# Kernel optimization log

Hardware: AMD Instinct MI355X
Metric: run time of the kernel (lower is better)

Reference implementation:

```python
import jax, jax.numpy as jnp
import numpy as np

B, T, D = 2, 2048, 1024
H = 16
HD = D // H
SCALE = 1.0 / np.sqrt(HD).astype(np.float32)


def setup_inputs() -> dict:
    key = jax.random.key(0)
    ks = jax.random.split(key, 5)
    std = 1.0 / np.sqrt(D).astype(np.float32)
    x = jax.random.normal(ks[0], (B, T, D), dtype=jnp.float32)
    Wqkvt = jax.random.normal(ks[1], (D, 4 * D), dtype=jnp.float32) * std
    bqkvt = jax.random.normal(ks[2], (4 * D,), dtype=jnp.float32) * 0.02
    Wout = jax.random.normal(ks[3], (D, D), dtype=jnp.float32) * std
    bout = jax.random.normal(ks[4], (D,), dtype=jnp.float32) * 0.02
    return {"x": x, "Wqkvt": Wqkvt, "bqkvt": bqkvt, "Wout": Wout, "bout": bout}


def reference(x, Wqkvt, bqkvt, Wout, bout):
    b, t, d = x.shape
    # fused qkvt projection -> [B,T,4,H,HD]
    qkvt = (x @ Wqkvt + bqkvt).reshape(b, t, 4, H, HD)
    # -> [B,H,T,HD] each
    q, k, v, tt = [jnp.transpose(qkvt[:, :, i], (0, 2, 1, 3)) for i in range(4)]

    # standard dot-product scores [B,H,T,T]
    scores_dot = jnp.einsum('bhqd,bhkd->bhqk', q, k)
    # triplet term: (q*t) against cumsum over keys of (k*v)/sqrt(hd)
    kv = k * v * SCALE
    kv_cum = jnp.cumsum(kv, axis=2)  # causal prefix over key positions
    scores_trip = jnp.einsum('bhqd,bhkd->bhqk', q * tt, kv_cum)

    scores = (scores_dot + scores_trip) * SCALE
    causal = jnp.triu(jnp.ones((t, t), dtype=bool), k=1)
    scores = jnp.where(causal[None, None], -jnp.inf, scores)

    attn = jax.nn.softmax(scores, axis=-1)
    out = jnp.einsum('bhqk,bhkd->bhqd', attn, v)  # [B,H,T,HD]
    out = jnp.transpose(out, (0, 2, 1, 3)).reshape(b, t, d)
    return out @ Wout + bout
```

## Files before the change

### kernel.cpp

```cpp
#include <hip/hip_runtime.h>

#define T_SEQ 2048
#define D_MODEL 1024
#define NH 16
#define HD 64
#define BH_TOT 32
#define M_ROWS 4096
#define NT 32
#define SCALE 0.125f
#define BHT (BH_TOT * T_SEQ)
#define LOG2E 1.44269504f
#define TAU 2.885f

typedef _Float16 h8 __attribute__((ext_vector_type(8)));
typedef _Float16 h4 __attribute__((ext_vector_type(4)));
typedef float f32x4 __attribute__((ext_vector_type(4)));

__device__ __forceinline__ f32x4 mfma_h(h8 a, h8 b, f32x4 c) {
    return __builtin_amdgcn_mfma_f32_16x16x32_f16(a, b, c, 0, 0, 0);
}

__device__ __forceinline__ void gload16(const _Float16* g, _Float16* l) {
    __builtin_amdgcn_global_load_lds(
        (const __attribute__((address_space(1))) unsigned int*)g,
        (__attribute__((address_space(3))) unsigned int*)l, 16, 0, 0);
}

__global__ void k_convert(const float* __restrict__ in, _Float16* __restrict__ out, int n) {
    int i = (blockIdx.x * blockDim.x + threadIdx.x) * 4;
    if (i < n) {
        float4 v = *(const float4*)(in + i);
        h4 o;
        o[0] = (_Float16)v.x; o[1] = (_Float16)v.y;
        o[2] = (_Float16)v.z; o[3] = (_Float16)v.w;
        *(h4*)(out + i) = o;
    }
}

__global__ void k_transpose(const float* __restrict__ in, _Float16* __restrict__ out, int K, int N) {
    __shared__ float tile[32][33];
    int nb = blockIdx.x * 32, kb = blockIdx.y * 32;
    int tx = threadIdx.x & 31, ty = threadIdx.x >> 5;
    #pragma unroll
    for (int i = 0; i < 32; i += 8)
        tile[ty + i][tx] = in[(size_t)(kb + ty + i) * N + (nb + tx)];
    __syncthreads();
    #pragma unroll
    for (int i = 0; i < 32; i += 8)
        out[(size_t)(nb + ty + i) * K + (kb + tx)] = (_Float16)tile[tx][ty + i];
}

template<int MODE>
__launch_bounds__(256, 2)
__global__ void k_gemm(const _Float16* __restrict__ A, const _Float16* __restrict__ Bt,
                       int M, int N, int K, const float* __restrict__ bias,
                       _Float16* __restrict__ qo, _Float16* __restrict__ keo,
                       _Float16* __restrict__ vo, _Float16* __restrict__ vto,
                       _Float16* __restrict__ to, float* __restrict__ cOut)
{
    __shared__ __align__(16) _Float16 lA[2][128 * 64];
    __shared__ __align__(16) _Float16 lB[2][128 * 64];
    const int tid = threadIdx.x;
    const int wid = tid >> 6, lane = tid & 63, lrow = lane & 15, lg = lane >> 4;
    const int wm = wid >> 1, wn = wid & 1;
    const int m0 = blockIdx.x * 128, n0 = blockIdx.y * 128;

    f32x4 acc[4][4];
    #pragma unroll
    for (int i = 0; i < 4; i++)
        #pragma unroll
        for (int j = 0; j < 4; j++) acc[i][j] = (f32x4){0.f, 0.f, 0.f, 0.f};

    const int rin = lane >> 3, gcol = lane & 7;
    const int scol = (gcol ^ rin) * 8;
    const _Float16* gA = A + (size_t)(m0 + 32 * wid + rin) * K + scol;
    const _Float16* gB = Bt + (size_t)(n0 + 32 * wid + rin) * K + scol;

    const int r7 = lrow & 7;
    const int nk = K >> 6;

    #pragma unroll
    for (int i = 0; i < 4; i++) {
        gload16(gA + (size_t)(8 * i) * K, &lA[0][32 * wid * 64 + 8 * i * 64]);
        gload16(gB + (size_t)(8 * i) * K, &lB[0][32 * wid * 64 + 8 * i * 64]);
    }
    __syncthreads();

    for (int kt = 0; kt < nk; ++kt) {
        const int cur = kt & 1;
        if (kt + 1 < nk) {
            const size_t ko = (size_t)(kt + 1) * 64;
            #pragma unroll
            for (int i = 0; i < 4; i++) {
                gload16(gA + (size_t)(8 * i) * K + ko, &lA[cur ^ 1][32 * wid * 64 + 8 * i * 64]);
                gload16(gB + (size_t)(8 * i) * K + ko, &lB[cur ^ 1][32 * wid * 64 + 8 * i * 64]);
            }
        }
        h8 af[4][2], bfr[4][2];
        #pragma unroll
        for (int mi = 0; mi < 4; mi++) {
            const int row = wm * 64 + mi * 16 + lrow;
            af[mi][0] = *(const h8*)&lA[cur][row * 64 + ((lg ^ r7) * 8)];
            af[mi][1] = *(const h8*)&lA[cur][row * 64 + (((4 + lg) ^ r7) * 8)];
        }
        #pragma unroll
        for (int ni = 0; ni < 4; ni++) {
            const int row = wn * 64 + ni * 16 + lrow;
            bfr[ni][0] = *(const h8*)&lB[cur][row * 64 + ((lg ^ r7) * 8)];
            bfr[ni][1] = *(const h8*)&lB[cur][row * 64 + (((4 + lg) ^ r7) * 8)];
        }
        #pragma unroll
        for (int mi = 0; mi < 4; mi++)
            #pragma unroll
            for (int ni = 0; ni < 4; ni++) {
                acc[mi][ni] = mfma_h(af[mi][0], bfr[ni][0], acc[mi][ni]);
                acc[mi][ni] = mfma_h(af[mi][1], bfr[ni][1], acc[mi][ni]);
            }
        __syncthreads();
    }

    if (MODE == 0) {
        const int ssel = n0 >> 10;
        #pragma unroll
        for (int mi = 0; mi < 4; mi++) {
            #pragma unroll
            for (int ni = 0; ni < 4; ni++) {
                const int nn = n0 + wn * 64 + ni * 16 + lrow;
                const float bv = bias[nn];
                const int h = (nn >> 6) & 15, hd = nn & 63;
                const int mmb = m0 + wm * 64 + mi * 16 + 4 * lg;
                const int b = mmb >> 11, t0 = mmb & (T_SEQ - 1);
                const size_t rowb = (size_t)(b * NH + h) * T_SEQ;
                h4 hv;
                #pragma unroll
                for (int r = 0; r < 4; r++) hv[r] = (_Float16)(acc[mi][ni][r] + bv);
                if (ssel == 0) {
                    #pragma unroll
                    for (int r = 0; r < 4; r++) qo[(rowb + t0 + r) * HD + hd] = hv[r];
                } else if (ssel == 1) {
                    #pragma unroll
                    for (int r = 0; r < 4; r++) keo[(rowb + t0 + r) * 128 + hd] = hv[r];
                } else if (ssel == 2) {
                    #pragma unroll
                    for (int r = 0; r < 4; r++) vo[(rowb + t0 + r) * HD + hd] = hv[r];
                    *(h4*)&vto[((size_t)(b * NH + h) * HD + hd) * T_SEQ + t0] = hv;
                } else {
                    #pragma unroll
                    for (int r = 0; r < 4; r++) to[(rowb + t0 + r) * HD + hd] = hv[r];
                }
            }
        }
    } else {
        #pragma unroll
        for (int mi = 0; mi < 4; mi++) {
            #pragma unroll
            for (int ni = 0; ni < 4; ni++) {
                const int nn = n0 + wn * 64 + ni * 16 + lrow;
                const float bv = bias[nn];
                #pragma unroll
                for (int r = 0; r < 4; r++) {
                    const int mm = m0 + wm * 64 + mi * 16 + 4 * lg + r;
                    cOut[(size_t)mm * N + nn] = acc[mi][ni][r] + bv;
                }
            }
        }
    }
}

__global__ void k_kvcum(_Float16* __restrict__ Ke, const _Float16* __restrict__ Vb)
{
    const int bh = blockIdx.x;
    const int w = threadIdx.x >> 6, lane = threadIdx.x & 63;
    const size_t bk = (size_t)bh * T_SEQ * 128 + lane;
    const size_t bv = (size_t)bh * T_SEQ * HD + lane;
    const int CH = T_SEQ / 16;
    const int t0 = w * CH;
    float s = 0.f;
    for (int i = 0; i < CH; i++)
        s += (float)Ke[bk + (size_t)(t0 + i) * 128] * (float)Vb[bv + (size_t)(t0 + i) * HD];
    __shared__ float tot[16][64];
    tot[w][lane] = s;
    __syncthreads();
    float acc = 0.f;
    for (int ww = 0; ww < w; ww++) acc += tot[ww][lane];
    for (int i = 0; i < CH; i++) {
        size_t ok = bk + (size_t)(t0 + i) * 128;
        acc += (float)Ke[ok] * (float)Vb[bv + (size_t)(t0 + i) * HD];
        Ke[ok + 64] = (_Float16)(acc * SCALE);
    }
}

__launch_bounds__(256, 2)
__global__ void k_attn(const _Float16* __restrict__ Qb, const _Float16* __restrict__ Ke,
                       const _Float16* __restrict__ Vt, const _Float16* __restrict__ Tb,
                       _Float16* __restrict__ Op0, _Float16* __restrict__ Op1,
                       _Float16* __restrict__ Op2, _Float16* __restrict__ Op3,
                       float* __restrict__ ML, int nsplit)
{
    const int bh = blockIdx.x;
    const int pair = blockIdx.y;
    const int ksel = blockIdx.z;
    const int tid = threadIdx.x;
    const int wid = tid >> 6, lane = tid & 63, lrow = lane & 15, lg = lane >> 4;
    const _Float16* qp = Qb + (size_t)bh * T_SEQ * HD;
    const _Float16* kep = Ke + (size_t)bh * T_SEQ * 128;
    const _Float16* tp = Tb + (size_t)bh * T_SEQ * HD;
    const _Float16* vp = Vt + (size_t)bh * T_SEQ * HD;
    _Float16* op = (ksel == 0) ? Op0 : (ksel == 1) ? Op1 : (ksel == 2) ? Op2 : Op3;
    float* ml = ML + (size_t)ksel * BHT * 2;

    __shared__ __align__(16) _Float16 ldsK[2][64 * 128];
    __shared__ __align__(16) _Float16 ldsV[2][64 * 64];
    __shared__ __align__(16) _Float16 lP[4][16 * 64];

    const int r7 = lrow & 7;
    int kswz[4];
    #pragma unroll
    for (int c = 0; c < 4; c++) kswz[c] = ((c * 4 + lg) ^ r7) * 8;

    const int krow4 = lane >> 4, kg = lane & 15;
    const int vrow8 = lane >> 3, vg = lane & 7;
    auto stage = [&](int j, int buf) {
        #pragma unroll
        for (int rr = 0; rr < 4; rr++) {
            const int row = 16 * wid + rr * 4 + krow4;
            gload16(&kep[(size_t)(j * 64 + row) * 128 + ((kg ^ (row & 7)) * 8)],
                    &ldsK[buf][(16 * wid + rr * 4) * 128]);
        }
        #pragma unroll
        for (int rr = 0; rr < 2; rr++) {
            const int d = 16 * wid + rr * 8 + vrow8;
            gload16(&vp[(size_t)d * T_SEQ + j * 64 + ((vg ^ (d & 7)) * 8)],
                    &ldsV[buf][(16 * wid + rr * 8) * 64]);
        }
    };

    const h8 ones = {(_Float16)1.f, (_Float16)1.f, (_Float16)1.f, (_Float16)1.f,
                     (_Float16)1.f, (_Float16)1.f, (_Float16)1.f, (_Float16)1.f};
    const float C = SCALE * LOG2E;

    for (int half = 0; half < 2; ++half) {
        const int qi = half ? (NT - 1 - pair) : pair;
        const int q0 = qi * 64;
        const int nj = qi + 1;
        const int jbeg = (nj * ksel) / nsplit;
        const int jend = (nj * (ksel + 1)) / nsplit;

        const int qrow = q0 + wid * 16 + lrow;
        h8 qf[4];
        #pragma unroll
        for (int ks = 0; ks < 2; ++ks) {
            h8 qv = *(const h8*)&qp[(size_t)qrow * HD + ks * 32 + lg * 8];
            h8 tv = *(const h8*)&tp[(size_t)qrow * HD + ks * 32 + lg * 8];
            h8 a2, b2;
            #pragma unroll
            for (int i = 0; i < 8; i++) {
                float qq = (float)qv[i] * C;
                a2[i] = (_Float16)qq;
                b2[i] = (_Float16)(qq * (float)tv[i]);
            }
            qf[ks] = a2; qf[2 + ks] = b2;
        }

        float m_r[4];
        f32x4 o[4], o4;
        #pragma unroll
        for (int r = 0; r < 4; r++) m_r[r] = -__builtin_inff();
        #pragma unroll
        for (int ct = 0; ct < 4; ct++) o[ct] = (f32x4){0.f, 0.f, 0.f, 0.f};
        o4 = (f32x4){0.f, 0.f, 0.f, 0.f};

        if (jbeg < jend) stage(jbeg, 0);
        __syncthreads();

        for (int j = jbeg; j < jend; ++j) {
            const int cur = (j - jbeg) & 1;
            if (j + 1 < jend) stage(j + 1, cur ^ 1);

            f32x4 s[4];
            #pragma unroll
            for (int ct = 0; ct < 4; ct++) {
                const _Float16* kb = &ldsK[cur][(ct * 16 + lrow) * 128];
                f32x4 sv = (f32x4){0.f, 0.f, 0.f, 0.f};
                sv = mfma_h(qf[0], *(const h8*)&kb[kswz[0]], sv);
                sv = mfma_h(qf[1], *(const h8*)&kb[kswz[1]], sv);
                sv = mfma_h(qf[2], *(const h8*)&kb[kswz[2]], sv);
                sv = mfma_h(qf[3], *(const h8*)&kb[kswz[3]], sv);
                s[ct] = sv;
            }
            if (j == qi) {
                #pragma unroll
                for (int ct = 0; ct < 4; ct++)
                    #pragma unroll
                    for (int r = 0; r < 4; r++) {
                        int key = j * 64 + ct * 16 + lrow;
                        int qr  = q0 + wid * 16 + 4 * lg + r;
                        if (key > qr) s[ct][r] = -__builtin_inff();
                    }
            }
            float mx[4];
            #pragma unroll
            for (int r = 0; r < 4; r++)
                mx[r] = fmaxf(fmaxf(s[0][r], s[1][r]), fmaxf(s[2][r], s[3][r]));
            bool need = (mx[0] > m_r[0] + TAU) | (mx[1] > m_r[1] + TAU) |
                        (mx[2] > m_r[2] + TAU) | (mx[3] > m_r[3] + TAU);
            if (__any(need)) {
                #pragma unroll
                for (int d = 1; d < 16; d <<= 1)
                    #pragma unroll
                    for (int r = 0; r < 4; r++) mx[r] = fmaxf(mx[r], __shfl_xor(mx[r], d, 64));
                #pragma unroll
                for (int r = 0; r < 4; r++) {
                    float mn = fmaxf(m_r[r], mx[r]);
                    float scl = __builtin_amdgcn_exp2f(m_r[r] - mn);
                    o[0][r] *= scl; o[1][r] *= scl; o[2][r] *= scl; o[3][r] *= scl;
                    o4[r] *= scl;
                    m_r[r] = mn;
                }
            }
            #pragma unroll
            for (int ct = 0; ct < 4; ct++) {
                const int col = ct * 16 + lrow;
                #pragma unroll
                for (int r = 0; r < 4; r++) {
                    float p = __builtin_amdgcn_exp2f(s[ct][r] - m_r[r]);
                    const int row = 4 * lg + r;
                    const int boff = row * 128 + ((col * 2) ^ ((row & 7) << 4));
                    lP[wid][boff >> 1] = (_Float16)p;
                }
            }
            h8 pa[2];
            #pragma unroll
            for (int ks = 0; ks < 2; ks++) {
                const int boff = lrow * 128 + ((ks * 64 + lg * 16) ^ ((lrow & 7) << 4));
                pa[ks] = *(const h8*)((const char*)lP[wid] + boff);
            }
            o4 = mfma_h(pa[0], ones, o4);
            o4 = mfma_h(pa[1], ones, o4);
            #pragma unroll
            for (int ct = 0; ct < 4; ct++) {
                const _Float16* vb = &ldsV[cur][(ct * 16 + lrow) * 64];
                o[ct] = mfma_h(pa[0], *(const h8*)&vb[kswz[0]], o[ct]);
                o[ct] = mfma_h(pa[1], *(const h8*)&vb[kswz[1]], o[ct]);
            }
            __syncthreads();
        }
        #pragma unroll
        for (int ct = 0; ct < 4; ct++)
            #pragma unroll
            for (int r = 0; r < 4; r++) {
                const int trow = q0 + wid * 16 + 4 * lg + r;
                const int d = ct * 16 + lrow;
                op[((size_t)bh * T_SEQ + trow) * HD + d] = (_Float16)o[ct][r];
            }
        if (lrow == 0) {
            #pragma unroll
            for (int r = 0; r < 4; r++) {
                const int trow = q0 + wid * 16 + 4 * lg + r;
                const size_t mi = ((size_t)bh * T_SEQ + trow) * 2;
                ml[mi] = m_r[r];
                ml[mi + 1] = o4[r];
            }
        }
    }
}

__global__ void k_combine(const _Float16* __restrict__ Op0, const _Float16* __restrict__ Op1,
                          const _Float16* __restrict__ Op2, const _Float16* __restrict__ Op3,
                          const float* __restrict__ ML, _Float16* __restrict__ AO, int nsplit)
{
    const int idx = blockIdx.x * 256 + threadIdx.x;
    const int row = idx >> 3;
    const int d0 = (idx & 7) * 8;
    const int bh = row >> 11, t = row & (T_SEQ - 1);
    const int b = bh >> 4, h = bh & 15;
    const _Float16* ops[4] = {Op0, Op1, Op2, Op3};
    float m = -__builtin_inff();
    for (int c = 0; c < nsplit; c++) m = fmaxf(m, ML[(size_t)c * BHT * 2 + 2 * row]);
    float w[4], denom = 0.f;
    for (int c = 0; c < nsplit; c++) {
        w[c] = __builtin_amdgcn_exp2f(ML[(size_t)c * BHT * 2 + 2 * row] - m);
        denom += w[c] * ML[(size_t)c * BHT * 2 + 2 * row + 1];
    }
    const float inv = 1.0f / denom;
    float accv[8];
    #pragma unroll
    for (int i = 0; i < 8; i++) accv[i] = 0.f;
    for (int c = 0; c < nsplit; c++) {
        h8 a = *(const h8*)&ops[c][(size_t)row * HD + d0];
        #pragma unroll
        for (int i = 0; i < 8; i++) accv[i] += w[c] * (float)a[i];
    }
    h8 r;
    #pragma unroll
    for (int i = 0; i < 8; i++) r[i] = (_Float16)(accv[i] * inv);
    *(h8*)&AO[((size_t)(b * T_SEQ + t)) * D_MODEL + h * HD + d0] = r;
}

extern "C" void kernel_launch(void* const* d_in, const int* in_sizes, int n_in,
                              void* d_out, int out_size, void* d_ws, size_t ws_size,
                              hipStream_t stream)
{
    const float* x     = (const float*)d_in[0];
    const float* Wqkvt = (const float*)d_in[1];
    const float* bqkvt = (const float*)d_in[2];
    const float* Wout  = (const float*)d_in[3];
    const float* bout  = (const float*)d_in[4];
    float* out = (float*)d_out;

    char* ws = (char*)d_ws;
    size_t off = 0;
    auto alloc = [&](size_t bytes) {
        char* p = ws + off;
        off += (bytes + 255) & ~(size_t)255;
        return p;
    };
    const size_t SZ = (size_t)M_ROWS * D_MODEL * 2;
    _Float16* xb  = (_Float16*)alloc(SZ);
    _Float16* wt  = (_Float16*)alloc(SZ);
    _Float16* wo  = (_Float16*)alloc((size_t)D_MODEL * D_MODEL * 2);
    _Float16* Qh  = (_Float16*)alloc(SZ);
    _Float16* Ke  = (_Float16*)alloc(SZ * 2);
    _Float16* Vh  = (_Float16*)alloc(SZ);
    _Float16* Vth = (_Float16*)alloc(SZ);
    _Float16* Th  = (_Float16*)alloc(SZ);
    _Float16* AO  = (_Float16*)alloc(SZ);
    const size_t need4 = off + 2 * SZ;
    _Float16* Op2 = (_Float16*)alloc(SZ);
    _Float16* Op3 = (_Float16*)alloc(SZ);

    const int nsplit = (ws_size >= need4) ? 4 : 2;

    _Float16* Op0 = xb;
    _Float16* Op1 = Vh;
    float*    ML  = (float*)wt;

    k_convert<<<4096, 256, 0, stream>>>(x, xb, M_ROWS * D_MODEL);
    k_transpose<<<dim3(128, 32), 256, 0, stream>>>(Wqkvt, wt, D_MODEL, 4 * D_MODEL);
    k_transpose<<<dim3(32, 32), 256, 0, stream>>>(Wout, wo, D_MODEL, D_MODEL);
    k_gemm<0><<<dim3(32, 32), 256, 0, stream>>>(xb, wt, M_ROWS, 4 * D_MODEL, D_MODEL,
                                                bqkvt, Qh, Ke, Vh, Vth, Th, nullptr);
    k_kvcum<<<BH_TOT, 1024, 0, stream>>>(Ke, Vh);
    k_attn<<<dim3(BH_TOT, NT / 2, nsplit), 256, 0, stream>>>(Qh, Ke, Vth, Th,
                                                             Op0, Op1, Op2, Op3, ML, nsplit);
    k_combine<<<BHT * HD / 8 / 256, 256, 0, stream>>>(Op0, Op1, Op2, Op3, ML, AO, nsplit);
    k_gemm<1><<<dim3(32, 8), 256, 0, stream>>>(AO, wo, M_ROWS, D_MODEL, D_MODEL,
                                               bout, nullptr, nullptr, nullptr, nullptr,
                                               nullptr, out);
}
```

Before: 190.8 us.

## Store K/V in MFMA-fragment order and read them directly from global in attention

The QKV GEMM epilogue and the kv-cumsum kernel now write K, cumulative KV and V into a pre-swizzled fragment layout, so each lane's h8 operand is one contiguous 16-byte global load. The attention kernel drops its LDS staging of K/V, the double buffer and the per-iteration barrier, and raises launch bounds to 4 blocks per SM. The P-tile LDS swizzle gets an extra XOR term to cut bank conflicts. The trade is that reuse moves from LDS to L2/L1: each wave loads the same K/V fragments on its own, and nothing prefetches the next tile.

After: 187.5 us. Within noise of the previous version (-1.7%).

```diff
diff --git a/kernel.cpp b/kernel.cpp
--- a/kernel.cpp
+++ b/kernel.cpp
@@ -54,9 +54,10 @@
 __launch_bounds__(256, 2)
 __global__ void k_gemm(const _Float16* __restrict__ A, const _Float16* __restrict__ Bt,
                        int M, int N, int K, const float* __restrict__ bias,
-                       _Float16* __restrict__ qo, _Float16* __restrict__ keo,
-                       _Float16* __restrict__ vo, _Float16* __restrict__ vto,
-                       _Float16* __restrict__ to, float* __restrict__ cOut)
+                       _Float16* __restrict__ qo, _Float16* __restrict__ kho,
+                       _Float16* __restrict__ kfo, _Float16* __restrict__ vo,
+                       _Float16* __restrict__ vfo, _Float16* __restrict__ to,
+                       float* __restrict__ cOut)
 {
     __shared__ __align__(16) _Float16 lA[2][128 * 64];
     __shared__ __align__(16) _Float16 lB[2][128 * 64];
@@ -130,7 +131,8 @@
                 const int h = (nn >> 6) & 15, hd = nn & 63;
                 const int mmb = m0 + wm * 64 + mi * 16 + 4 * lg;
                 const int b = mmb >> 11, t0 = mmb & (T_SEQ - 1);
-                const size_t rowb = (size_t)(b * NH + h) * T_SEQ;
+                const int bh = b * NH + h;
+                const size_t rowb = (size_t)bh * T_SEQ;
                 h4 hv;
                 #pragma unroll
                 for (int r = 0; r < 4; r++) hv[r] = (_Float16)(acc[mi][ni][r] + bv);
@@ -138,12 +140,22 @@
                     #pragma unroll
                     for (int r = 0; r < 4; r++) qo[(rowb + t0 + r) * HD + hd] = hv[r];
                 } else if (ssel == 1) {
-                    #pragma unroll
-                    for (int r = 0; r < 4; r++) keo[(rowb + t0 + r) * 128 + hd] = hv[r];
+                    const int ksK = hd >> 5, lgK = (hd & 31) >> 3, iK = hd & 7;
+                    #pragma unroll
+                    for (int r = 0; r < 4; r++) {
+                        const int t = t0 + r;
+                        kho[(rowb + t) * HD + hd] = hv[r];
+                        const int j = t >> 6, ct = (t >> 4) & 3;
+                        const int laneF = (t & 15) | (lgK << 4);
+                        kfo[(((size_t)bh * 32 + j) * 16 + ct * 4 + ksK) * 512 + laneF * 8 + iK] = hv[r];
+                    }
                 } else if (ssel == 2) {
                     #pragma unroll
                     for (int r = 0; r < 4; r++) vo[(rowb + t0 + r) * HD + hd] = hv[r];
-                    *(h4*)&vto[((size_t)(b * NH + h) * HD + hd) * T_SEQ + t0] = hv;
+                    const int ctV = hd >> 4, lrV = hd & 15;
+                    const int j = t0 >> 6, ksV = (t0 >> 5) & 1, lgV = (t0 >> 3) & 3, i0 = t0 & 7;
+                    const int laneF = lrV | (lgV << 4);
+                    *(h4*)&vfo[(((size_t)bh * 32 + j) * 8 + ctV * 2 + ksV) * 512 + laneF * 8 + i0] = hv;
                 } else {
                     #pragma unroll
                     for (int r = 0; r < 4; r++) to[(rowb + t0 + r) * HD + hd] = hv[r];
@@ -167,32 +179,39 @@
     }
 }
 
-__global__ void k_kvcum(_Float16* __restrict__ Ke, const _Float16* __restrict__ Vb)
+__global__ void k_kvcum(const _Float16* __restrict__ Kh, const _Float16* __restrict__ Vh,
+                        _Float16* __restrict__ KF)
 {
     const int bh = blockIdx.x;
-    const int w = threadIdx.x >> 6, lane = threadIdx.x & 63;
-    const size_t bk = (size_t)bh * T_SEQ * 128 + lane;
-    const size_t bv = (size_t)bh * T_SEQ * HD + lane;
+    const int w = threadIdx.x >> 6, d = threadIdx.x & 63;
+    const size_t base = (size_t)bh * T_SEQ * HD + d;
     const int CH = T_SEQ / 16;
     const int t0 = w * CH;
     float s = 0.f;
-    for (int i = 0; i < CH; i++)
-        s += (float)Ke[bk + (size_t)(t0 + i) * 128] * (float)Vb[bv + (size_t)(t0 + i) * HD];
+    for (int i = 0; i < CH; i++) {
+        size_t o = base + (size_t)(t0 + i) * HD;
+        s += (float)Kh[o] * (float)Vh[o];
+    }
     __shared__ float tot[16][64];
-    tot[w][lane] = s;
+    tot[w][d] = s;
     __syncthreads();
     float acc = 0.f;
-    for (int ww = 0; ww < w; ww++) acc += tot[ww][lane];
+    for (int ww = 0; ww < w; ww++) acc += tot[ww][d];
+    const int ksK = 2 + (d >> 5), lgK = (d & 31) >> 3, iK = d & 7;
     for (int i = 0; i < CH; i++) {
-        size_t ok = bk + (size_t)(t0 + i) * 128;
-        acc += (float)Ke[ok] * (float)Vb[bv + (size_t)(t0 + i) * HD];
-        Ke[ok + 64] = (_Float16)(acc * SCALE);
-    }
-}
-
-__launch_bounds__(256, 2)
-__global__ void k_attn(const _Float16* __restrict__ Qb, const _Float16* __restrict__ Ke,
-                       const _Float16* __restrict__ Vt, const _Float16* __restrict__ Tb,
+        const int t = t0 + i;
+        size_t o = base + (size_t)t * HD;
+        acc += (float)Kh[o] * (float)Vh[o];
+        const int j = t >> 6, ct = (t >> 4) & 3;
+        const int laneF = (t & 15) | (lgK << 4);
+        KF[(((size_t)bh * 32 + j) * 16 + ct * 4 + ksK) * 512 + laneF * 8 + iK] =
+            (_Float16)(acc * SCALE);
+    }
+}
+
+__launch_bounds__(256, 4)
+__global__ void k_attn(const _Float16* __restrict__ Qb, const _Float16* __restrict__ Tb,
+                       const _Float16* __restrict__ KF, const _Float16* __restrict__ VF,
                        _Float16* __restrict__ Op0, _Float16* __restrict__ Op1,
                        _Float16* __restrict__ Op2, _Float16* __restrict__ Op3,
                        float* __restrict__ ML, int nsplit)
@@ -203,37 +222,13 @@
     const int tid = threadIdx.x;
     const int wid = tid >> 6, lane = tid & 63, lrow = lane & 15, lg = lane >> 4;
     const _Float16* qp = Qb + (size_t)bh * T_SEQ * HD;
-    const _Float16* kep = Ke + (size_t)bh * T_SEQ * 128;
     const _Float16* tp = Tb + (size_t)bh * T_SEQ * HD;
-    const _Float16* vp = Vt + (size_t)bh * T_SEQ * HD;
+    const _Float16* kfb = KF + (size_t)bh * 32 * 16 * 512;
+    const _Float16* vfb = VF + (size_t)bh * 32 * 8 * 512;
     _Float16* op = (ksel == 0) ? Op0 : (ksel == 1) ? Op1 : (ksel == 2) ? Op2 : Op3;
     float* ml = ML + (size_t)ksel * BHT * 2;
 
-    __shared__ __align__(16) _Float16 ldsK[2][64 * 128];
-    __shared__ __align__(16) _Float16 ldsV[2][64 * 64];
     __shared__ __align__(16) _Float16 lP[4][16 * 64];
-
-    const int r7 = lrow & 7;
-    int kswz[4];
-    #pragma unroll
-    for (int c = 0; c < 4; c++) kswz[c] = ((c * 4 + lg) ^ r7) * 8;
-
-    const int krow4 = lane >> 4, kg = lane & 15;
-    const int vrow8 = lane >> 3, vg = lane & 7;
-    auto stage = [&](int j, int buf) {
-        #pragma unroll
-        for (int rr = 0; rr < 4; rr++) {
-            const int row = 16 * wid + rr * 4 + krow4;
-            gload16(&kep[(size_t)(j * 64 + row) * 128 + ((kg ^ (row & 7)) * 8)],
-                    &ldsK[buf][(16 * wid + rr * 4) * 128]);
-        }
-        #pragma unroll
-        for (int rr = 0; rr < 2; rr++) {
-            const int d = 16 * wid + rr * 8 + vrow8;
-            gload16(&vp[(size_t)d * T_SEQ + j * 64 + ((vg ^ (d & 7)) * 8)],
-                    &ldsV[buf][(16 * wid + rr * 8) * 64]);
-        }
-    };
 
     const h8 ones = {(_Float16)1.f, (_Float16)1.f, (_Float16)1.f, (_Float16)1.f,
                      (_Float16)1.f, (_Float16)1.f, (_Float16)1.f, (_Float16)1.f};
@@ -270,22 +265,16 @@
         for (int ct = 0; ct < 4; ct++) o[ct] = (f32x4){0.f, 0.f, 0.f, 0.f};
         o4 = (f32x4){0.f, 0.f, 0.f, 0.f};
 
-        if (jbeg < jend) stage(jbeg, 0);
-        __syncthreads();
-
         for (int j = jbeg; j < jend; ++j) {
-            const int cur = (j - jbeg) & 1;
-            if (j + 1 < jend) stage(j + 1, cur ^ 1);
-
             f32x4 s[4];
             #pragma unroll
             for (int ct = 0; ct < 4; ct++) {
-                const _Float16* kb = &ldsK[cur][(ct * 16 + lrow) * 128];
+                const _Float16* kb = kfb + ((size_t)j * 16 + ct * 4) * 512 + lane * 8;
                 f32x4 sv = (f32x4){0.f, 0.f, 0.f, 0.f};
-                sv = mfma_h(qf[0], *(const h8*)&kb[kswz[0]], sv);
-                sv = mfma_h(qf[1], *(const h8*)&kb[kswz[1]], sv);
-                sv = mfma_h(qf[2], *(const h8*)&kb[kswz[2]], sv);
-                sv = mfma_h(qf[3], *(const h8*)&kb[kswz[3]], sv);
+                sv = mfma_h(qf[0], *(const h8*)kb, sv);
+                sv = mfma_h(qf[1], *(const h8*)(kb + 512), sv);
+                sv = mfma_h(qf[2], *(const h8*)(kb + 1024), sv);
+                sv = mfma_h(qf[3], *(const h8*)(kb + 1536), sv);
                 s[ct] = sv;
             }
             if (j == qi) {
@@ -325,25 +314,25 @@
                 for (int r = 0; r < 4; r++) {
                     float p = __builtin_amdgcn_exp2f(s[ct][r] - m_r[r]);
                     const int row = 4 * lg + r;
-                    const int boff = row * 128 + ((col * 2) ^ ((row & 7) << 4));
+                    const int boff = row * 128 + ((col * 2) ^ ((row & 7) << 4) ^ ((row & 12) << 3));
                     lP[wid][boff >> 1] = (_Float16)p;
                 }
             }
             h8 pa[2];
             #pragma unroll
             for (int ks = 0; ks < 2; ks++) {
-                const int boff = lrow * 128 + ((ks * 64 + lg * 16) ^ ((lrow & 7) << 4));
+                const int boff = lrow * 128 +
+                    ((ks * 64 + lg * 16) ^ ((lrow & 7) << 4) ^ ((lrow & 12) << 3));
                 pa[ks] = *(const h8*)((const char*)lP[wid] + boff);
             }
             o4 = mfma_h(pa[0], ones, o4);
             o4 = mfma_h(pa[1], ones, o4);
             #pragma unroll
             for (int ct = 0; ct < 4; ct++) {
-                const _Float16* vb = &ldsV[cur][(ct * 16 + lrow) * 64];
-                o[ct] = mfma_h(pa[0], *(const h8*)&vb[kswz[0]], o[ct]);
-                o[ct] = mfma_h(pa[1], *(const h8*)&vb[kswz[1]], o[ct]);
-            }
-            __syncthreads();
+                const _Float16* vb = vfb + ((size_t)j * 8 + ct * 2) * 512 + lane * 8;
+                o[ct] = mfma_h(pa[0], *(const h8*)vb, o[ct]);
+                o[ct] = mfma_h(pa[1], *(const h8*)(vb + 512), o[ct]);
+            }
         }
         #pragma unroll
         for (int ct = 0; ct < 4; ct++)
@@ -420,31 +409,32 @@
     _Float16* wt  = (_Float16*)alloc(SZ);
     _Float16* wo  = (_Float16*)alloc((size_t)D_MODEL * D_MODEL * 2);
     _Float16* Qh  = (_Float16*)alloc(SZ);
-    _Float16* Ke  = (_Float16*)alloc(SZ * 2);
+    _Float16* Kh  = (_Float16*)alloc(SZ);
     _Float16* Vh  = (_Float16*)alloc(SZ);
-    _Float16* Vth = (_Float16*)alloc(SZ);
     _Float16* Th  = (_Float16*)alloc(SZ);
+    _Float16* KF  = (_Float16*)alloc(SZ * 2);
+    _Float16* VF  = (_Float16*)alloc(SZ);
     _Float16* AO  = (_Float16*)alloc(SZ);
-    const size_t need4 = off + 2 * SZ;
-    _Float16* Op2 = (_Float16*)alloc(SZ);
     _Float16* Op3 = (_Float16*)alloc(SZ);
+    const size_t need4 = off;
 
     const int nsplit = (ws_size >= need4) ? 4 : 2;
 
     _Float16* Op0 = xb;
     _Float16* Op1 = Vh;
+    _Float16* Op2 = Kh;
     float*    ML  = (float*)wt;
 
     k_convert<<<4096, 256, 0, stream>>>(x, xb, M_ROWS * D_MODEL);
     k_transpose<<<dim3(128, 32), 256, 0, stream>>>(Wqkvt, wt, D_MODEL, 4 * D_MODEL);
     k_transpose<<<dim3(32, 32), 256, 0, stream>>>(Wout, wo, D_MODEL, D_MODEL);
     k_gemm<0><<<dim3(32, 32), 256, 0, stream>>>(xb, wt, M_ROWS, 4 * D_MODEL, D_MODEL,
-                                                bqkvt, Qh, Ke, Vh, Vth, Th, nullptr);
-    k_kvcum<<<BH_TOT, 1024, 0, stream>>>(Ke, Vh);
-    k_attn<<<dim3(BH_TOT, NT / 2, nsplit), 256, 0, stream>>>(Qh, Ke, Vth, Th,
+                                                bqkvt, Qh, Kh, KF, Vh, VF, Th, nullptr);
+    k_kvcum<<<BH_TOT, 1024, 0, stream>>>(Kh, Vh, KF);
+    k_attn<<<dim3(BH_TOT, NT / 2, nsplit), 256, 0, stream>>>(Qh, Th, KF, VF,
                                                              Op0, Op1, Op2, Op3, ML, nsplit);
     k_combine<<<BHT * HD / 8 / 256, 256, 0, stream>>>(Op0, Op1, Op2, Op3, ML, AO, nsplit);
     k_gemm<1><<<dim3(32, 8), 256, 0, stream>>>(AO, wo, M_ROWS, D_MODEL, D_MODEL,
                                                bout, nullptr, nullptr, nullptr, nullptr,
-                                               nullptr, out);
-}
+                                               nullptr, nullptr, out);
+}
```
